# Kernel tuning notes

Hardware: AMD Instinct MI355X
Metric: run time of the kernel (lower is better)

## Reference

```python
import jax, jax.numpy as jnp
import numpy as np

N = 100000       # nodes
E = 1600000      # edges (avg degree 16)
F_IN, H, C = 128, 128, 47


def setup_inputs() -> dict:
    key = jax.random.key(0)
    ks = jax.random.split(key, 12)
    def lin(k, fan_in, fan_out):
        return (jax.random.normal(k, (fan_in, fan_out), dtype=jnp.float32)
                / np.float32(np.sqrt(fan_in)))
    return {
        "x": jax.random.normal(ks[0], (N, F_IN), dtype=jnp.float32),
        "src": jax.random.randint(ks[1], (E,), 0, N, dtype=jnp.int32),
        "dst": jax.random.randint(ks[2], (E,), 0, N, dtype=jnp.int32),
        "w_self0": lin(ks[3], F_IN, H),
        "w_neigh0": lin(ks[4], F_IN, H),
        "b0": jnp.zeros((H,), jnp.float32),
        "w_self1": lin(ks[5], H, H),
        "w_neigh1": lin(ks[6], H, H),
        "b1": jnp.zeros((H,), jnp.float32),
        "w_self2": lin(ks[7], H, C),
        "w_neigh2": lin(ks[8], H, C),
        "b2": jnp.zeros((C,), jnp.float32),
    }


def _sage_layer(h, src, dst, w_self, w_neigh, b):
    # mean-aggregate neighbor features: gather h[src], scatter-add to dst
    agg = jax.ops.segment_sum(h[src], dst, num_segments=N)        # [N, d]
    deg = jax.ops.segment_sum(jnp.ones((src.shape[0], 1), h.dtype), dst,
                              num_segments=N)                     # [N, 1]
    mean = agg / jnp.maximum(deg, 1.0)
    # DGL SAGEConv('mean'): fc_self(h_dst) + fc_neigh(mean) + bias
    return h @ w_self + mean @ w_neigh + b


def reference(x, src, dst,
              w_self0, w_neigh0, b0,
              w_self1, w_neigh1, b1,
              w_self2, w_neigh2, b2):
    h = _sage_layer(x, src, dst, w_self0, w_neigh0, b0)
    h = jax.nn.relu(h)  # dropout is identity in eval mode
    h = _sage_layer(h, src, dst, w_self1, w_neigh1, b1)
    h = jax.nn.relu(h)
    h = _sage_layer(h, src, dst, w_self2, w_neigh2, b2)
    return h
```

## Files before the change

### kernel.cpp

```cpp
#include <hip/hip_runtime.h>

typedef unsigned int u32;
typedef unsigned short u16;
typedef __attribute__((ext_vector_type(8))) short short8;
typedef __attribute__((ext_vector_type(4))) float f32x4;

__device__ __forceinline__ u16 f2bf(float f) {
    u32 u = __float_as_uint(f);
    u32 r = (u + 0x7fffu + ((u >> 16) & 1u)) >> 16;
    return (u16)r;
}
__device__ __forceinline__ float bf2f(u32 lo16) { return __uint_as_float(lo16 << 16); }

__device__ __forceinline__ void acc_u4p(float2* a, uint4 v) {
    u32 w[4] = {v.x, v.y, v.z, v.w};
#pragma unroll
    for (int i = 0; i < 4; i++) {
        float2 t;
        t.x = __uint_as_float(w[i] << 16);
        t.y = __uint_as_float(w[i] & 0xffff0000u);
        a[i].x += t.x;
        a[i].y += t.y;
    }
}


__global__ __launch_bounds__(256) void prep_w_all(const float* __restrict__ ws0, const float* __restrict__ wn0, u16* __restrict__ wt0,
                                                  const float* __restrict__ ws1, const float* __restrict__ wn1, u16* __restrict__ wt1,
                                                  const float* __restrict__ ws2, const float* __restrict__ wn2, u16* __restrict__ wt2) {
    int bid = blockIdx.x;
    const float *ws, *wn;
    u16* wt;
    int dout, HW, local;
    if (bid < 128)      { ws = ws0; wn = wn0; wt = wt0; dout = 128; HW = 128; local = bid; }
    else if (bid < 256) { ws = ws1; wn = wn1; wt = wt1; dout = 128; HW = 128; local = bid - 128; }
    else                { ws = ws2; wn = wn2; wt = wt2; dout = 47;  HW = 64;  local = bid - 256; }
    int idx = local * 256 + threadIdx.x;
    int n = idx >> 7, k = idx & 127;
    float v = 0.f;
    if (n < HW) { if (n < dout) v = ws[k * dout + n]; }
    else { int nn = n - HW; if (nn < dout) v = wn[k * dout + nn]; }
    wt[idx] = f2bf(v);
}


__global__ __launch_bounds__(256) void hist_k(const int* __restrict__ dst,
                                              int* __restrict__ deg, int E) {
    int i = blockIdx.x * 256 + threadIdx.x;
    if (i < E) atomicAdd(&deg[dst[i]], 1);
}

__global__ __launch_bounds__(256) void scan_partial(const int* __restrict__ deg,
                                                    int* __restrict__ bsum, int Nn) {
    __shared__ int sm[256];
    int t = threadIdx.x;
    int base = blockIdx.x * 1024 + t * 4;
    int s = 0;
#pragma unroll
    for (int j = 0; j < 4; j++)
        if (base + j < Nn) s += deg[base + j];
    sm[t] = s;
    __syncthreads();
    for (int off = 128; off > 0; off >>= 1) {
        if (t < off) sm[t] += sm[t + off];
        __syncthreads();
    }
    if (t == 0) bsum[blockIdx.x] = sm[0];
}

__global__ __launch_bounds__(256) void scan_offsets(const int* __restrict__ bsum,
                                                    int* __restrict__ boff, int nb) {
    __shared__ int sm[256];
    int t = threadIdx.x;
    int v = (t < nb) ? bsum[t] : 0;
    sm[t] = v;
    __syncthreads();
    for (int off = 1; off < 256; off <<= 1) {
        int u = (t >= off) ? sm[t - off] : 0;
        __syncthreads();
        sm[t] += u;
        __syncthreads();
    }
    if (t < nb) boff[t] = sm[t] - v;
}

__global__ __launch_bounds__(1024) void scan_final(const int* __restrict__ deg,
                                                   const int* __restrict__ boff,
                                                   int* __restrict__ rowptr,
                                                   float* __restrict__ invd,
                                                   int* __restrict__ cursor,
                                                   int Nn, int E) {
    __shared__ int sm[1024];
    int t = threadIdx.x;
    int i = blockIdx.x * 1024 + t;
    int v = (i < Nn) ? deg[i] : 0;
    sm[t] = v;
    __syncthreads();
    for (int off = 1; off < 1024; off <<= 1) {
        int u = (t >= off) ? sm[t - off] : 0;
        __syncthreads();
        sm[t] += u;
        __syncthreads();
    }
    if (i < Nn) {
        int rp = boff[blockIdx.x] + sm[t] - v;
        rowptr[i] = rp;
        invd[i] = 1.0f / (float)max(v, 1);
        if ((i & 511) == 0) cursor[i >> 9] = rp;
    }
    if (i == Nn) rowptr[Nn] = E;
}

#define TILE 4096
__global__ __launch_bounds__(512) void bucket_scatter(const int* __restrict__ src,
                                                      const int* __restrict__ dst,
                                                      int* __restrict__ cursor,
                                                      uint2* __restrict__ pairs, int E) {
    __shared__ uint2 sp[TILE];
    __shared__ int s_cnt[256], s_off[256], s_gpos[256], s_cnt2[256];
    const int tid = threadIdx.x;
    const int base = blockIdx.x * TILE;
    const int tn = min(TILE, E - base);
    if (tid < 256) { s_cnt[tid] = 0; s_cnt2[tid] = 0; }
    __syncthreads();
    int d[8], s[8];
#pragma unroll
    for (int j = 0; j < 8; j++) {
        int k = tid + j * 512;
        if (k < tn) {
            d[j] = dst[base + k];
            s[j] = src[base + k];
            atomicAdd(&s_cnt[d[j] >> 9], 1);
        } else d[j] = -1;
    }
    __syncthreads();
    if (tid < 256) s_off[tid] = s_cnt[tid];
    __syncthreads();
    for (int off = 1; off < 256; off <<= 1) {
        int v = 0;
        if (tid < 256 && tid >= off) v = s_off[tid - off];
        __syncthreads();
        if (tid < 256) s_off[tid] += v;
        __syncthreads();
    }
    if (tid < 256 && s_cnt[tid] > 0) s_gpos[tid] = atomicAdd(&cursor[tid], s_cnt[tid]);
    __syncthreads();
#pragma unroll
    for (int j = 0; j < 8; j++) {
        if (d[j] >= 0) {
            int b = d[j] >> 9;
            int p = atomicAdd(&s_cnt2[b], 1);
            sp[s_off[b] - s_cnt[b] + p] = make_uint2((u32)d[j], (u32)s[j]);
        }
    }
    __syncthreads();
    for (int k = tid; k < tn; k += 512) {
        uint2 pr = sp[k];
        int b = (int)(pr.x >> 9);
        pairs[s_gpos[b] + (k - (s_off[b] - s_cnt[b]))] = pr;
    }
}

#define LDSCAP 12288
__global__ __launch_bounds__(512) void build_csr(const uint2* __restrict__ pairs,
                                                 const int* __restrict__ rowptr,
                                                 int* __restrict__ cols, int Nn) {
    __shared__ int s_cols[LDSCAP];
    __shared__ int s_row[513];
    __shared__ int s_cnt[512];
    const int tid = threadIdx.x;
    const int d0 = blockIdx.x * 512;
    const int nd = min(512, Nn - d0);
    for (int i = tid; i <= nd; i += 512) s_row[i] = rowptr[d0 + i];
    if (tid < nd) s_cnt[tid] = 0;
    __syncthreads();
    const int base = s_row[0];
    const int n = s_row[nd] - base;
    const bool fit = (n <= LDSCAP);
    for (int k = tid; k < n; k += 512) {
        uint2 pr = pairs[base + k];
        int dl = (int)pr.x - d0;
        int p = atomicAdd(&s_cnt[dl], 1);
        int pos = s_row[dl] - base + p;
        if (fit) s_cols[pos] = (int)pr.y;
        else cols[base + pos] = (int)pr.y;
    }
    __syncthreads();
    if (fit)
        for (int k = tid; k < n; k += 512) cols[base + k] = s_cols[k];
}

#define KDIM 128
#define KP 136

template <int NCOLS, bool AF32>
__global__ __launch_bounds__(256) void gemm_bf16(const void* __restrict__ Ap,
                                                 const u16* __restrict__ Bt,
                                                 u16* __restrict__ C, int M) {
    __shared__ u16 As[64 * KP];
    __shared__ u16 Bs[128 * KP];
    const int row0 = blockIdx.x * 64;
    const int col0 = blockIdx.y * 128;
    const int tid = threadIdx.x;

#pragma unroll
    for (int i = 0; i < 4; i++) {
        int idx = tid + i * 256;
        int r = idx >> 4, c = idx & 15;
        uint4 v = make_uint4(0, 0, 0, 0);
        if (row0 + r < M) {
            if (AF32) {
                const float* Af = (const float*)Ap;
                const float4* rowp = (const float4*)(Af + (size_t)(row0 + r) * KDIM);
                float4 f0 = rowp[2 * c];
                float4 f1 = rowp[2 * c + 1];
                v.x = (u32)f2bf(f0.x) | ((u32)f2bf(f0.y) << 16);
                v.y = (u32)f2bf(f0.z) | ((u32)f2bf(f0.w) << 16);
                v.z = (u32)f2bf(f1.x) | ((u32)f2bf(f1.y) << 16);
                v.w = (u32)f2bf(f1.z) | ((u32)f2bf(f1.w) << 16);
            } else {
                const u16* Ab = (const u16*)Ap;
                v = ((const uint4*)(Ab + (size_t)(row0 + r) * KDIM))[c];
            }
        }
        ((uint4*)(As + r * KP))[c] = v;
    }
#pragma unroll
    for (int i = 0; i < 8; i++) {
        int idx = tid + i * 256;
        int r = idx >> 4, c = idx & 15;
        uint4 v = ((const uint4*)(Bt + (size_t)(col0 + r) * KDIM))[c];
        ((uint4*)(Bs + r * KP))[c] = v;
    }
    __syncthreads();

    const int lane = tid & 63, wave = tid >> 6;
    const int quad = lane >> 4, l16 = lane & 15;
    const int wcol = wave * 32;

    f32x4 acc[4][2];
#pragma unroll
    for (int mt = 0; mt < 4; mt++)
#pragma unroll
        for (int nt = 0; nt < 2; nt++) acc[mt][nt] = (f32x4){0.f, 0.f, 0.f, 0.f};

#pragma unroll
    for (int kc = 0; kc < 4; kc++) {
        short8 a[4], b[2];
#pragma unroll
        for (int mt = 0; mt < 4; mt++)
            a[mt] = *(const short8*)(As + (size_t)(mt * 16 + l16) * KP + kc * 32 + quad * 8);
#pragma unroll
        for (int nt = 0; nt < 2; nt++)
            b[nt] = *(const short8*)(Bs + (size_t)(wcol + nt * 16 + l16) * KP + kc * 32 + quad * 8);
#pragma unroll
        for (int mt = 0; mt < 4; mt++)
#pragma unroll
            for (int nt = 0; nt < 2; nt++)
                acc[mt][nt] = __builtin_amdgcn_mfma_f32_16x16x32_bf16(a[mt], b[nt], acc[mt][nt], 0, 0, 0);
    }

    __syncthreads();
#pragma unroll
    for (int mt = 0; mt < 4; mt++)
#pragma unroll
        for (int i = 0; i < 4; i++) {
            int rl = mt * 16 + quad * 4 + i;
#pragma unroll
            for (int nt = 0; nt < 2; nt++)
                As[rl * KP + wcol + nt * 16 + l16] = f2bf(acc[mt][nt][i]);
        }
    __syncthreads();
#pragma unroll
    for (int it = 0; it < 4; it++) {
        int idx = tid + it * 256;
        int r = idx >> 4, c8 = idx & 15;
        if (row0 + r < M)
            *(uint4*)(C + (size_t)(row0 + r) * NCOLS + col0 + c8 * 8) =
                *(const uint4*)(As + r * KP + c8 * 8);
    }
}

template <bool RELU>
__global__ __launch_bounds__(256) void agg128_k(const u16* __restrict__ out2,
                                                const int* __restrict__ rowptr,
                                                const int* __restrict__ cols,
                                                const float* __restrict__ invd,
                                                const float* __restrict__ bias,
                                                u16* __restrict__ outp, int Mn) {
    int wave = threadIdx.x >> 6, lane = threadIdx.x & 63;
    int node = blockIdx.x * 4 + wave;
    if (node >= Mn) return;
    int sub = lane >> 4, l16 = lane & 15;
    const u16* tb = out2 + 128 + 8 * l16;
    int beg = rowptr[node], end = rowptr[node + 1];
    float2 a[4];
#pragma unroll
    for (int i = 0; i < 4; i++) a[i] = make_float2(0.f, 0.f);
    int e = beg + sub;
    while (e < end) {
        int s0 = cols[e];
        int s1 = (e + 4  < end) ? cols[e + 4]  : Mn;
        int s2 = (e + 8  < end) ? cols[e + 8]  : Mn;
        int s3 = (e + 12 < end) ? cols[e + 12] : Mn;
        uint4 v0 = *(const uint4*)(tb + (size_t)s0 * 256);
        uint4 v1 = *(const uint4*)(tb + (size_t)s1 * 256);
        uint4 v2 = *(const uint4*)(tb + (size_t)s2 * 256);
        uint4 v3 = *(const uint4*)(tb + (size_t)s3 * 256);
        acc_u4p(a, v0); acc_u4p(a, v1); acc_u4p(a, v2); acc_u4p(a, v3);
        e += 16;
    }
    float af[8] = {a[0].x, a[0].y, a[1].x, a[1].y, a[2].x, a[2].y, a[3].x, a[3].y};
#pragma unroll
    for (int j = 0; j < 8; j++) {
        af[j] += __shfl_xor(af[j], 16); af[j] += __shfl_xor(af[j], 32);
    }
    if (sub == 0) {
        float id = invd[node];
        uint4 sv = *(const uint4*)(out2 + (size_t)node * 256 + 8 * l16);
        float4 b0 = *(const float4*)(bias + 8 * l16);
        float4 b1 = *(const float4*)(bias + 8 * l16 + 4);
        float o0 = bf2f(sv.x & 0xffffu) + af[0] * id + b0.x;
        float o1 = bf2f(sv.x >> 16)     + af[1] * id + b0.y;
        float o2 = bf2f(sv.y & 0xffffu) + af[2] * id + b0.z;
        float o3 = bf2f(sv.y >> 16)     + af[3] * id + b0.w;
        float o4 = bf2f(sv.z & 0xffffu) + af[4] * id + b1.x;
        float o5 = bf2f(sv.z >> 16)     + af[5] * id + b1.y;
        float o6 = bf2f(sv.w & 0xffffu) + af[6] * id + b1.z;
        float o7 = bf2f(sv.w >> 16)     + af[7] * id + b1.w;
        if (RELU) {
            o0 = fmaxf(o0, 0.f); o1 = fmaxf(o1, 0.f); o2 = fmaxf(o2, 0.f); o3 = fmaxf(o3, 0.f);
            o4 = fmaxf(o4, 0.f); o5 = fmaxf(o5, 0.f); o6 = fmaxf(o6, 0.f); o7 = fmaxf(o7, 0.f);
        }
        uint4 w;
        w.x = (u32)f2bf(o0) | ((u32)f2bf(o1) << 16);
        w.y = (u32)f2bf(o2) | ((u32)f2bf(o3) << 16);
        w.z = (u32)f2bf(o4) | ((u32)f2bf(o5) << 16);
        w.w = (u32)f2bf(o6) | ((u32)f2bf(o7) << 16);
        *(uint4*)(outp + (size_t)node * 128 + 8 * l16) = w;
    }
}

__global__ __launch_bounds__(256) void agg_out8_k(const u16* __restrict__ out2,
                                                  const int* __restrict__ rowptr,
                                                  const int* __restrict__ cols,
                                                  const float* __restrict__ invd,
                                                  const float* __restrict__ bias,
                                                  float* __restrict__ outp, int Mn) {
    int wave = threadIdx.x >> 6, lane = threadIdx.x & 63;
    int node = blockIdx.x * 4 + wave;
    if (node >= Mn) return;
    int e8 = lane >> 3, l8 = lane & 7;
    const u16* tb = out2 + 64 + 8 * l8;
    int beg = rowptr[node], end = rowptr[node + 1];
    float2 a[4];
#pragma unroll
    for (int i = 0; i < 4; i++) a[i] = make_float2(0.f, 0.f);
    int e = beg + e8;
    while (e < end) {
        int s0 = cols[e];
        int s1 = (e + 8  < end) ? cols[e + 8]  : Mn;
        int s2 = (e + 16 < end) ? cols[e + 16] : Mn;
        int s3 = (e + 24 < end) ? cols[e + 24] : Mn;
        uint4 v0 = *(const uint4*)(tb + (size_t)s0 * 128);
        uint4 v1 = *(const uint4*)(tb + (size_t)s1 * 128);
        uint4 v2 = *(const uint4*)(tb + (size_t)s2 * 128);
        uint4 v3 = *(const uint4*)(tb + (size_t)s3 * 128);
        acc_u4p(a, v0); acc_u4p(a, v1); acc_u4p(a, v2); acc_u4p(a, v3);
        e += 32;
    }
    float af[8] = {a[0].x, a[0].y, a[1].x, a[1].y, a[2].x, a[2].y, a[3].x, a[3].y};
#pragma unroll
    for (int j = 0; j < 8; j++) {
        af[j] += __shfl_xor(af[j], 8); af[j] += __shfl_xor(af[j], 16); af[j] += __shfl_xor(af[j], 32);
    }
    if (e8 == 0) {
        float id = invd[node];
        uint4 sv = *(const uint4*)(out2 + (size_t)node * 128 + 8 * l8);
        u32 sw[4] = {sv.x, sv.y, sv.z, sv.w};
        float* orow = outp + (size_t)node * 47;
#pragma unroll
        for (int j = 0; j < 8; j++) {
            int c = 8 * l8 + j;
            if (c < 47) {
                float s = bf2f((j & 1) ? (sw[j >> 1] >> 16) : (sw[j >> 1] & 0xffffu));
                orow[c] = s + af[j] * id + bias[c];
            }
        }
    }
}


extern "C" void kernel_launch(void* const* d_in, const int* in_sizes, int n_in,
                              void* d_out, int out_size, void* d_ws, size_t ws_size,
                              hipStream_t stream) {
    const float* x   = (const float*)d_in[0];
    const int*   src = (const int*)d_in[1];
    const int*   dst = (const int*)d_in[2];
    const float* ws0 = (const float*)d_in[3];
    const float* wn0 = (const float*)d_in[4];
    const float* b0  = (const float*)d_in[5];
    const float* ws1 = (const float*)d_in[6];
    const float* wn1 = (const float*)d_in[7];
    const float* b1  = (const float*)d_in[8];
    const float* ws2 = (const float*)d_in[9];
    const float* wn2 = (const float*)d_in[10];
    const float* b2  = (const float*)d_in[11];

    const int Nn = in_sizes[0] / 128;
    const int E  = in_sizes[1];

    char* p = (char*)d_ws;
    auto alloc = [&](size_t bytes) -> void* {
        void* r = (void*)p;
        p += (bytes + 255) & ~(size_t)255;
        return r;
    };
    u16*   bufA   = (u16*)alloc((size_t)Nn * 128 * 2);
    u16*   out2   = (u16*)alloc(((size_t)Nn * 256 + 256) * 2);
    u16*   wt0    = (u16*)alloc(256 * 128 * 2);
    u16*   wt1    = (u16*)alloc(256 * 128 * 2);
    u16*   wt2    = (u16*)alloc(128 * 128 * 2);
    int*   deg    = (int*)alloc((size_t)Nn * 4);
    int*   rowptr = (int*)alloc((size_t)(Nn + 1) * 4);
    float* invd   = (float*)alloc((size_t)Nn * 4);
    int*   cols   = (int*)alloc((size_t)(E + 32) * 4);
    int*   bsum   = (int*)alloc(256 * 4);
    int*   boff   = (int*)alloc(256 * 4);
    int*   cursor = (int*)alloc(256 * 4);
    uint2* pairs  = (uint2*)out2;

    hipMemsetAsync(deg, 0, (size_t)Nn * 4, stream);
    hipMemsetAsync(out2 + (size_t)Nn * 256, 0, 512, stream);

    prep_w_all<<<320, 256, 0, stream>>>(ws0, wn0, wt0, ws1, wn1, wt1, ws2, wn2, wt2);

    hist_k<<<(E + 255) / 256, 256, 0, stream>>>(dst, deg, E);
    const int nb = (Nn + 1023) / 1024;
    const int nb2 = (Nn + 1 + 1023) / 1024;
    scan_partial<<<nb, 256, 0, stream>>>(deg, bsum, Nn);
    scan_offsets<<<1, 256, 0, stream>>>(bsum, boff, nb);
    scan_final<<<nb2, 1024, 0, stream>>>(deg, boff, rowptr, invd, cursor, Nn, E);

    bucket_scatter<<<(E + TILE - 1) / TILE, 512, 0, stream>>>(src, dst, cursor, pairs, E);
    build_csr<<<(Nn + 511) / 512, 512, 0, stream>>>(pairs, rowptr, cols, Nn);

    dim3 ggrid((Nn + 63) / 64, 2);
    dim3 ggrid1((Nn + 63) / 64, 1);
    const int aggGrid = (Nn + 3) / 4;
    gemm_bf16<256, true><<<ggrid, 256, 0, stream>>>(x, wt0, out2, Nn);
    agg128_k<true><<<aggGrid, 256, 0, stream>>>(out2, rowptr, cols, invd, b0, bufA, Nn);
    gemm_bf16<256, false><<<ggrid, 256, 0, stream>>>(bufA, wt1, out2, Nn);
    agg128_k<true><<<aggGrid, 256, 0, stream>>>(out2, rowptr, cols, invd, b1, bufA, Nn);
    gemm_bf16<128, false><<<ggrid1, 256, 0, stream>>>(bufA, wt2, out2, Nn);
    hipMemsetAsync(out2 + (size_t)Nn * 128, 0, 256, stream);
    agg_out8_k<<<aggGrid, 256, 0, stream>>>(out2, rowptr, cols, invd, b2, (float*)d_out, Nn);
}
```

Measured before the change: 451.7 us.

## Replace per-node degree histogram with bucket histogram and per-bucket local scan

Result: faster. 393.8 us (-12.8%).

```diff
diff --git a/kernel.cpp b/kernel.cpp
--- a/kernel.cpp
+++ b/kernel.cpp
@@ -44,35 +44,35 @@
 }
 
 
-__global__ __launch_bounds__(256) void hist_k(const int* __restrict__ dst,
-                                              int* __restrict__ deg, int E) {
-    int i = blockIdx.x * 256 + threadIdx.x;
-    if (i < E) atomicAdd(&deg[dst[i]], 1);
-}
-
-__global__ __launch_bounds__(256) void scan_partial(const int* __restrict__ deg,
-                                                    int* __restrict__ bsum, int Nn) {
+__global__ __launch_bounds__(256) void hist256(const int* __restrict__ dst,
+                                               int* __restrict__ bcnt, int E) {
+    __shared__ int bins[256];
+    bins[threadIdx.x] = 0;
+    __syncthreads();
+    int gid = blockIdx.x * 256 + threadIdx.x;
+    int stride = gridDim.x * 256;
+    const int4* d4 = (const int4*)dst;
+    int n4 = E >> 2;
+    for (int k = gid; k < n4; k += stride) {
+        int4 v = d4[k];
+        atomicAdd(&bins[v.x >> 9], 1);
+        atomicAdd(&bins[v.y >> 9], 1);
+        atomicAdd(&bins[v.z >> 9], 1);
+        atomicAdd(&bins[v.w >> 9], 1);
+    }
+    for (int k = (n4 << 2) + gid; k < E; k += stride)
+        atomicAdd(&bins[dst[k] >> 9], 1);
+    __syncthreads();
+    int b = bins[threadIdx.x];
+    if (b) atomicAdd(&bcnt[threadIdx.x], b);
+}
+
+__global__ __launch_bounds__(256) void scan256(const int* __restrict__ bcnt,
+                                               int* __restrict__ boff,
+                                               int* __restrict__ cursor) {
     __shared__ int sm[256];
     int t = threadIdx.x;
-    int base = blockIdx.x * 1024 + t * 4;
-    int s = 0;
-#pragma unroll
-    for (int j = 0; j < 4; j++)
-        if (base + j < Nn) s += deg[base + j];
-    sm[t] = s;
-    __syncthreads();
-    for (int off = 128; off > 0; off >>= 1) {
-        if (t < off) sm[t] += sm[t + off];
-        __syncthreads();
-    }
-    if (t == 0) bsum[blockIdx.x] = sm[0];
-}
-
-__global__ __launch_bounds__(256) void scan_offsets(const int* __restrict__ bsum,
-                                                    int* __restrict__ boff, int nb) {
-    __shared__ int sm[256];
-    int t = threadIdx.x;
-    int v = (t < nb) ? bsum[t] : 0;
+    int v = bcnt[t];
     sm[t] = v;
     __syncthreads();
     for (int off = 1; off < 256; off <<= 1) {
@@ -81,34 +81,10 @@
         sm[t] += u;
         __syncthreads();
     }
-    if (t < nb) boff[t] = sm[t] - v;
-}
-
-__global__ __launch_bounds__(1024) void scan_final(const int* __restrict__ deg,
-                                                   const int* __restrict__ boff,
-                                                   int* __restrict__ rowptr,
-                                                   float* __restrict__ invd,
-                                                   int* __restrict__ cursor,
-                                                   int Nn, int E) {
-    __shared__ int sm[1024];
-    int t = threadIdx.x;
-    int i = blockIdx.x * 1024 + t;
-    int v = (i < Nn) ? deg[i] : 0;
-    sm[t] = v;
-    __syncthreads();
-    for (int off = 1; off < 1024; off <<= 1) {
-        int u = (t >= off) ? sm[t - off] : 0;
-        __syncthreads();
-        sm[t] += u;
-        __syncthreads();
-    }
-    if (i < Nn) {
-        int rp = boff[blockIdx.x] + sm[t] - v;
-        rowptr[i] = rp;
-        invd[i] = 1.0f / (float)max(v, 1);
-        if ((i & 511) == 0) cursor[i >> 9] = rp;
-    }
-    if (i == Nn) rowptr[Nn] = E;
+    int excl = sm[t] - v;
+    boff[t] = excl;
+    cursor[t] = excl;
+    if (t == 255) boff[256] = sm[255];
 }
 
 #define TILE 4096
@@ -162,32 +138,65 @@
 }
 
 #define LDSCAP 12288
-__global__ __launch_bounds__(512) void build_csr(const uint2* __restrict__ pairs,
-                                                 const int* __restrict__ rowptr,
-                                                 int* __restrict__ cols, int Nn) {
+__global__ __launch_bounds__(512) void build_csr2(const uint2* __restrict__ pairs,
+                                                  const int* __restrict__ boff,
+                                                  int* __restrict__ rowptr,
+                                                  float* __restrict__ invd,
+                                                  int* __restrict__ cols, int Nn, int E) {
+    __shared__ int s_pack[LDSCAP];
     __shared__ int s_cols[LDSCAP];
-    __shared__ int s_row[513];
     __shared__ int s_cnt[512];
+    __shared__ int s_off[512];
+    __shared__ int s_cnt2[512];
     const int tid = threadIdx.x;
     const int d0 = blockIdx.x * 512;
     const int nd = min(512, Nn - d0);
-    for (int i = tid; i <= nd; i += 512) s_row[i] = rowptr[d0 + i];
-    if (tid < nd) s_cnt[tid] = 0;
-    __syncthreads();
-    const int base = s_row[0];
-    const int n = s_row[nd] - base;
+    const int base = boff[blockIdx.x];
+    const int n = boff[blockIdx.x + 1] - base;
     const bool fit = (n <= LDSCAP);
+    s_cnt[tid] = 0; s_cnt2[tid] = 0;
+    __syncthreads();
     for (int k = tid; k < n; k += 512) {
         uint2 pr = pairs[base + k];
         int dl = (int)pr.x - d0;
-        int p = atomicAdd(&s_cnt[dl], 1);
-        int pos = s_row[dl] - base + p;
-        if (fit) s_cols[pos] = (int)pr.y;
-        else cols[base + pos] = (int)pr.y;
-    }
-    __syncthreads();
-    if (fit)
+        atomicAdd(&s_cnt[dl], 1);
+        if (fit) s_pack[k] = (dl << 17) | (int)pr.y;
+    }
+    __syncthreads();
+    int v = s_cnt[tid];
+    s_off[tid] = v;
+    __syncthreads();
+    for (int off = 1; off < 512; off <<= 1) {
+        int u = (tid >= off) ? s_off[tid - off] : 0;
+        __syncthreads();
+        s_off[tid] += u;
+        __syncthreads();
+    }
+    int excl = s_off[tid] - v;
+    if (tid < nd) {
+        rowptr[d0 + tid] = base + excl;
+        invd[d0 + tid] = 1.0f / (float)max(v, 1);
+    }
+    if (blockIdx.x == 0 && tid == 0) rowptr[Nn] = E;
+    s_off[tid] = excl;
+    __syncthreads();
+    if (fit) {
+        for (int k = tid; k < n; k += 512) {
+            int pk = s_pack[k];
+            int dl = pk >> 17;
+            int p = atomicAdd(&s_cnt2[dl], 1);
+            s_cols[s_off[dl] + p] = pk & 0x1ffff;
+        }
+        __syncthreads();
         for (int k = tid; k < n; k += 512) cols[base + k] = s_cols[k];
+    } else {
+        for (int k = tid; k < n; k += 512) {
+            uint2 pr = pairs[base + k];
+            int dl = (int)pr.x - d0;
+            int p = atomicAdd(&s_cnt2[dl], 1);
+            cols[base + s_off[dl] + p] = (int)pr.y;
+        }
+    }
 }
 
 #define KDIM 128
@@ -421,29 +430,24 @@
     u16*   wt0    = (u16*)alloc(256 * 128 * 2);
     u16*   wt1    = (u16*)alloc(256 * 128 * 2);
     u16*   wt2    = (u16*)alloc(128 * 128 * 2);
-    int*   deg    = (int*)alloc((size_t)Nn * 4);
     int*   rowptr = (int*)alloc((size_t)(Nn + 1) * 4);
     float* invd   = (float*)alloc((size_t)Nn * 4);
     int*   cols   = (int*)alloc((size_t)(E + 32) * 4);
-    int*   bsum   = (int*)alloc(256 * 4);
-    int*   boff   = (int*)alloc(256 * 4);
+    int*   bcnt   = (int*)alloc(256 * 4);
+    int*   boff   = (int*)alloc(257 * 4);
     int*   cursor = (int*)alloc(256 * 4);
     uint2* pairs  = (uint2*)out2;
 
-    hipMemsetAsync(deg, 0, (size_t)Nn * 4, stream);
+    hipMemsetAsync(bcnt, 0, 256 * 4, stream);
     hipMemsetAsync(out2 + (size_t)Nn * 256, 0, 512, stream);
 
     prep_w_all<<<320, 256, 0, stream>>>(ws0, wn0, wt0, ws1, wn1, wt1, ws2, wn2, wt2);
 
-    hist_k<<<(E + 255) / 256, 256, 0, stream>>>(dst, deg, E);
-    const int nb = (Nn + 1023) / 1024;
-    const int nb2 = (Nn + 1 + 1023) / 1024;
-    scan_partial<<<nb, 256, 0, stream>>>(deg, bsum, Nn);
-    scan_offsets<<<1, 256, 0, stream>>>(bsum, boff, nb);
-    scan_final<<<nb2, 1024, 0, stream>>>(deg, boff, rowptr, invd, cursor, Nn, E);
+    hist256<<<512, 256, 0, stream>>>(dst, bcnt, E);
+    scan256<<<1, 256, 0, stream>>>(bcnt, boff, cursor);
 
     bucket_scatter<<<(E + TILE - 1) / TILE, 512, 0, stream>>>(src, dst, cursor, pairs, E);
-    build_csr<<<(Nn + 511) / 512, 512, 0, stream>>>(pairs, rowptr, cols, Nn);
+    build_csr2<<<(Nn + 511) / 512, 512, 0, stream>>>(pairs, boff, rowptr, invd, cols, Nn, E);
 
     dim3 ggrid((Nn + 63) / 64, 2);
     dim3 ggrid1((Nn + 63) / 64, 1);
```
